# Kernel optimization log

Hardware: AMD Instinct MI355X
Metric: run time of the kernel (lower is better)

The kernel has to match this reference:

```python
import jax, jax.numpy as jnp
import numpy as np

SIGMA = 1.0          # from global `args.sigma` in the original repo
ALPHA = 0.99         # self.alpha
TOPK = 4             # torch.topk(W, 4)
NUM_CLASSES = 2
EPS = float(np.finfo(float).eps)


def setup_inputs() -> dict:
    key = jax.random.key(0)
    k1, k2, k3 = jax.random.split(key, 3)
    labeled_inputs = jax.random.normal(k1, (1024, 1024), dtype=jnp.float32)
    labeled_target = jax.random.randint(k2, (1024,), 0, NUM_CLASSES, dtype=jnp.int64)
    unlabeled_inputs = jax.random.normal(k3, (3072, 1024), dtype=jnp.float32)
    return {"labeled_inputs": labeled_inputs,
            "labeled_target": labeled_target,
            "unlabeled_inputs": unlabeled_inputs}


def _label_prop(labeled_inputs, unlabeled_inputs, labeled_target):
    num_support = labeled_inputs.shape[0]
    emb_all = jnp.concatenate([labeled_inputs, unlabeled_inputs], axis=0)  # [N, d]
    N, d = emb_all.shape

    # mean_j (x_i - x_k)_j^2 = (|x_i|^2 + |x_k|^2 - 2 x_i.x_k) / d
    # (algebraically identical to the torch NxNxd broadcast, without materializing it)
    sq = jnp.sum(emb_all * emb_all, axis=1)                 # [N]
    dist = (sq[:, None] + sq[None, :] - 2.0 * (emb_all @ emb_all.T)) / d
    W = jnp.exp(-dist / (2.0 * SIGMA * SIGMA))              # [N, N]

    # zero the diagonal
    eye = jnp.eye(N, dtype=W.dtype)
    W = W * (1.0 - eye)

    # top-k per row -> symmetric binary mask
    _, indices = jax.lax.top_k(W, TOPK)                     # [N, k]
    mask = jnp.zeros_like(W)
    rows = jnp.arange(N)[:, None]
    mask = mask.at[rows, indices].set(1.0)
    mask = ((mask + mask.T) > 0).astype(jnp.float32)
    W = W * mask

    # symmetric degree normalization S = D^{-1/2} W D^{-1/2}
    D = W.sum(axis=0)                                       # [N]
    D_sqrt_inv = jnp.sqrt(1.0 / (D + EPS))
    S = D_sqrt_inv[:, None] * W * D_sqrt_inv[None, :]

    # labels: one-hot support, zeros for queries
    ys = jax.nn.one_hot(labeled_target, NUM_CLASSES, dtype=jnp.float32)
    yu = jnp.zeros((N - num_support, NUM_CLASSES), dtype=jnp.float32)
    y = jnp.concatenate([ys, yu], axis=0)                   # [N, C]

    # F = (I - alpha*S + eps)^{-1} y   (solve == inverse @ y)
    A = jnp.eye(N, dtype=jnp.float32) - ALPHA * S + EPS
    Fk = jnp.linalg.solve(A, y)
    return Fk[num_support:, :]                              # [num_queries, C]


def reference(labeled_inputs, labeled_target, unlabeled_inputs):
    return _label_prop(labeled_inputs, unlabeled_inputs, labeled_target)
```

## Files before the change

kernel.cpp:

```cpp
#include <hip/hip_runtime.h>

#define N_ALL 4096
#define N_LAB 1024
#define DIMF 1024
#define EDGECAP 32768
#define ALPHA_ 0.99f
#define NIT_CH 100
#define EPS_D 2.220446049250313e-16

typedef short bf16x8 __attribute__((ext_vector_type(8)));
typedef float f32x4 __attribute__((ext_vector_type(4)));

struct __align__(8) Edge { unsigned j; float w; };

__device__ inline const float* xrow(const float* L, const float* U, int r) {
  return (r < N_LAB) ? (L + (size_t)r * DIMF) : (U + (size_t)(r - N_LAB) * DIMF);
}

__device__ inline void load_lds16(const void* g, void* l) {
  __builtin_amdgcn_global_load_lds(
      (const __attribute__((address_space(1))) unsigned int*)g,
      (__attribute__((address_space(3))) unsigned int*)l, 16, 0, 0);
}

__device__ inline unsigned short bf16rne(float f) {
  unsigned u = __float_as_uint(f);
  unsigned r = (u + 0x7fffu + ((u >> 16) & 1u)) >> 16;
  return (unsigned short)r;
}

__global__ __launch_bounds__(256) void labfmt_k(const int* __restrict__ lab,
                                                int* __restrict__ flag) {
  const long long* l64 = (const long long*)lab;
  int bad = 0;
  for (int k = threadIdx.x; k < 512; k += 256) {
    long long v = l64[k];
    if (v != 0 && v != 1) bad = 1;
  }
  __shared__ int sbad[4];
  unsigned long long m = __ballot(bad);
  if ((threadIdx.x & 63) == 0) sbad[threadIdx.x >> 6] = (m != 0ull);
  __syncthreads();
  if (threadIdx.x == 0)
    flag[0] = (sbad[0] | sbad[1] | sbad[2] | sbad[3]) ? 0 : 1;
}

__global__ __launch_bounds__(256) void prep_k(const float* __restrict__ L,
                                              const float* __restrict__ U,
                                              unsigned short* __restrict__ Xbf,
                                              float* __restrict__ sq,
                                              double* __restrict__ sqd) {
  const int row = blockIdx.x;
  const int tid = threadIdx.x;
  const float* src = xrow(L, U, row);
  float4 v = ((const float4*)src)[tid];
  ushort4 h;
  h.x = bf16rne(v.x); h.y = bf16rne(v.y); h.z = bf16rne(v.z); h.w = bf16rne(v.w);
  ((ushort4*)(Xbf + (size_t)row * DIMF))[tid] = h;
  float s = v.x * v.x + v.y * v.y + v.z * v.z + v.w * v.w;
  double sd = (double)v.x * v.x + (double)v.y * v.y +
              (double)v.z * v.z + (double)v.w * v.w;
#pragma unroll
  for (int d = 32; d >= 1; d >>= 1) {
    s += __shfl_xor(s, d);
    sd += __shfl_xor(sd, d);
  }
  __shared__ float wsum[4];
  __shared__ double wsumd[4];
  if ((tid & 63) == 0) { wsum[tid >> 6] = s; wsumd[tid >> 6] = sd; }
  __syncthreads();
  if (tid == 0) {
    sq[row] = wsum[0] + wsum[1] + wsum[2] + wsum[3];
    sqd[row] = wsumd[0] + wsumd[1] + wsumd[2] + wsumd[3];
  }
}

__global__ __launch_bounds__(256) void gemm_w(const unsigned short* __restrict__ Xbf,
                                              const float* __restrict__ sq,
                                              float* __restrict__ W) {
  __shared__ unsigned short At[128 * 32];
  __shared__ unsigned short Bt[128 * 32];
  const int tid = threadIdx.x;
  const int wave = tid >> 6, lane = tid & 63;
  const int brow = blockIdx.y * 128, bcol = blockIdx.x * 128;
  const int q = lane >> 4, rl = lane & 15;
  const int wr = (wave >> 1) * 64, wc = (wave & 1) * 64;

  f32x4 acc[4][4] = {};

  const int srow = tid >> 2;
  const int soff = (tid & 3) * 8;

  for (int k0 = 0; k0 < DIMF; k0 += 32) {
#pragma unroll
    for (int half = 0; half < 2; ++half) {
      const unsigned short* ga =
          Xbf + (size_t)(brow + half * 64 + srow) * DIMF + k0 + soff;
      load_lds16(ga, &At[(half * 64 + wave * 16) * 32]);
      const unsigned short* gb =
          Xbf + (size_t)(bcol + half * 64 + srow) * DIMF + k0 + soff;
      load_lds16(gb, &Bt[(half * 64 + wave * 16) * 32]);
    }
    __syncthreads();
    bf16x8 af[4], bf_[4];
#pragma unroll
    for (int t = 0; t < 4; ++t) {
      af[t] = *(const bf16x8*)&At[(wr + t * 16 + rl) * 32 + q * 8];
      bf_[t] = *(const bf16x8*)&Bt[(wc + t * 16 + rl) * 32 + q * 8];
    }
#pragma unroll
    for (int i = 0; i < 4; ++i)
#pragma unroll
      for (int j = 0; j < 4; ++j)
        acc[i][j] = __builtin_amdgcn_mfma_f32_16x16x32_bf16(af[i], bf_[j], acc[i][j], 0, 0, 0);
    __syncthreads();
  }

#pragma unroll
  for (int i = 0; i < 4; ++i) {
#pragma unroll
    for (int j = 0; j < 4; ++j) {
#pragma unroll
      for (int reg = 0; reg < 4; ++reg) {
        int gr = brow + wr + i * 16 + q * 4 + reg;
        int gc = bcol + wc + j * 16 + rl;
        float g = acc[i][j][reg];
        float dist = (sq[gr] + sq[gc] - 2.0f * g) * (1.0f / 1024.0f);
        float w = expf(-0.5f * dist);
        if (gr == gc) w = 0.0f;
        W[(size_t)gr * N_ALL + gc] = w;
      }
    }
  }
}

__global__ __launch_bounds__(256) void top8_k(const float* __restrict__ W,
                                              unsigned* __restrict__ t8i) {
  const int wave = threadIdx.x >> 6, lane = threadIdx.x & 63;
  const int row = blockIdx.x * 4 + wave;
  const float* Wr = W + (size_t)row * N_ALL;
  float bv[8]; unsigned bj[8];
#pragma unroll
  for (int t = 0; t < 8; ++t) { bv[t] = -1.0f; bj[t] = 0xFFFFFFFFu; }
  float minv = -1.0f; int mins = 0;
  for (int s = 0; s < 64; ++s) {
    int j = s * 64 + lane;
    float v = Wr[j];
    if (v > minv) {
#pragma unroll
      for (int t = 0; t < 8; ++t) if (t == mins) { bv[t] = v; bj[t] = (unsigned)j; }
      minv = bv[0]; mins = 0;
#pragma unroll
      for (int t = 1; t < 8; ++t) if (bv[t] < minv) { minv = bv[t]; mins = t; }
    }
  }
  for (int pick = 0; pick < 8; ++pick) {
    unsigned long long best = 0;
#pragma unroll
    for (int t = 0; t < 8; ++t) {
      bool valid = (bv[t] >= 0.0f);
      unsigned long long key =
          ((unsigned long long)__float_as_uint(bv[t]) << 32) |
          (unsigned long long)(0xFFFFFFFFu - bj[t]);
      if (valid && key > best) best = key;
    }
#pragma unroll
    for (int d = 32; d >= 1; d >>= 1) {
      unsigned long long o = __shfl_xor(best, d);
      if (o > best) best = o;
    }
    unsigned wj = 0xFFFFFFFFu - (unsigned)(best & 0xFFFFFFFFull);
    if (lane == 0) t8i[row * 8 + pick] = wj;
#pragma unroll
    for (int t = 0; t < 8; ++t) if (bj[t] == wj) bv[t] = -1.0f;
  }
}

__global__ __launch_bounds__(256) void rerank_k(const float* __restrict__ L,
                                                const float* __restrict__ U,
                                                const double* __restrict__ sqd,
                                                const unsigned* __restrict__ t8i,
                                                unsigned* __restrict__ t4i) {
  const int wave = threadIdx.x >> 6, lane = threadIdx.x & 63;
  const int row = blockIdx.x * 4 + wave;
  const float* xi = xrow(L, U, row);
  float xr[16];
#pragma unroll
  for (int t = 0; t < 16; ++t) xr[t] = xi[t * 64 + lane];
  unsigned cj[8];
  double cw[8];
#pragma unroll
  for (int c = 0; c < 8; ++c) cj[c] = t8i[row * 8 + c];
  for (int c = 0; c < 8; ++c) {
    const float* xj = xrow(L, U, (int)cj[c]);
    double s = 0.0;
#pragma unroll
    for (int t = 0; t < 16; ++t) s += (double)xr[t] * xj[t * 64 + lane];
#pragma unroll
    for (int d = 32; d >= 1; d >>= 1) s += __shfl_xor(s, d);
    double dist = (sqd[row] + sqd[cj[c]] - 2.0 * s) * (1.0 / 1024.0);
    cw[c] = exp(-0.5 * dist);
  }
  if (lane == 0) {
#pragma unroll
    for (int pick = 0; pick < 4; ++pick) {
      int ms = -1;
      double mv = -1.0;
      unsigned mj = 0xFFFFFFFFu;
#pragma unroll
      for (int c = 0; c < 8; ++c) {
        bool better = (cw[c] > mv) || (cw[c] == mv && cj[c] < mj);
        if (cw[c] >= 0.0 && better) { mv = cw[c]; mj = cj[c]; ms = c; }
      }
      t4i[row * 4 + pick] = mj;
      cw[ms] = -2.0;
    }
  }
}

__global__ __launch_bounds__(256) void cnt4_k(const unsigned* __restrict__ t4i,
                                              unsigned* __restrict__ nn) {
  const int wave = threadIdx.x >> 6, lane = threadIdx.x & 63;
  const int i = blockIdx.x * 4 + wave;
  const uint4 mine = ((const uint4*)t4i)[i];
  unsigned base = 0;
  for (int j0 = 0; j0 < N_ALL; j0 += 64) {
    int j = j0 + lane;
    uint4 tj = ((const uint4*)t4i)[j];
    bool keep = (mine.x == (unsigned)j) | (mine.y == (unsigned)j) |
                (mine.z == (unsigned)j) | (mine.w == (unsigned)j) |
                (tj.x == (unsigned)i) | (tj.y == (unsigned)i) |
                (tj.z == (unsigned)i) | (tj.w == (unsigned)i);
    keep = keep && (j != i);
    base += (unsigned)__popcll(__ballot(keep));
  }
  if (lane == 0) nn[i] = base;
}

__global__ __launch_bounds__(64) void scanP_k(const unsigned* __restrict__ nn,
                                              unsigned* __restrict__ rowPtr) {
  const int lane = threadIdx.x;
  unsigned running = 0;
  for (int j0 = 0; j0 < N_ALL; j0 += 64) {
    int v = (int)nn[j0 + lane];
    int incl = v;
#pragma unroll
    for (int d = 1; d < 64; d <<= 1) {
      int t = __shfl_up(incl, d);
      if (lane >= d) incl += t;
    }
    rowPtr[j0 + lane] = running + (unsigned)(incl - v);
    running += (unsigned)__shfl(incl, 63);
  }
  if (lane == 0) rowPtr[N_ALL] = running;
}

__global__ __launch_bounds__(256) void csrfill_k(const unsigned* __restrict__ t4i,
                                                 const unsigned* __restrict__ rowPtr,
                                                 Edge* __restrict__ edges,
                                                 unsigned* __restrict__ eRow) {
  const int wave = threadIdx.x >> 6, lane = threadIdx.x & 63;
  const int i = blockIdx.x * 4 + wave;
  const uint4 mine = ((const uint4*)t4i)[i];
  unsigned base = rowPtr[i];
  for (int j0 = 0; j0 < N_ALL; j0 += 64) {
    int j = j0 + lane;
    uint4 tj = ((const uint4*)t4i)[j];
    bool keep = (mine.x == (unsigned)j) | (mine.y == (unsigned)j) |
                (mine.z == (unsigned)j) | (mine.w == (unsigned)j) |
                (tj.x == (unsigned)i) | (tj.y == (unsigned)i) |
                (tj.z == (unsigned)i) | (tj.w == (unsigned)i);
    keep = keep && (j != i);
    unsigned long long m = __ballot(keep);
    if (keep) {
      unsigned pos = base + (unsigned)__popcll(m & ((1ull << lane) - 1ull));
      edges[pos].j = (unsigned)j;
      edges[pos].w = 0.0f;
      eRow[pos] = (unsigned)i;
    }
    base += (unsigned)__popcll(m);
  }
}

__global__ __launch_bounds__(256) void edgeval_k(const float* __restrict__ L,
                                                 const float* __restrict__ U,
                                                 const double* __restrict__ sqd,
                                                 const unsigned* __restrict__ rowPtr,
                                                 const unsigned* __restrict__ eRow,
                                                 Edge* __restrict__ edges) {
  const int wave = threadIdx.x >> 6, lane = threadIdx.x & 63;
  const unsigned e = blockIdx.x * 4 + wave;
  if (e >= rowPtr[N_ALL]) return;
  const unsigned i = eRow[e];
  const unsigned j = edges[e].j;
  const float* xi = xrow(L, U, (int)i);
  const float* xj = xrow(L, U, (int)j);
  double s = 0.0;
#pragma unroll
  for (int t = 0; t < 16; ++t)
    s += (double)xi[t * 64 + lane] * xj[t * 64 + lane];
#pragma unroll
  for (int d = 32; d >= 1; d >>= 1) s += __shfl_xor(s, d);
  if (lane == 0) {
    double dist = (sqd[i] + sqd[j] - 2.0 * s) * (1.0 / 1024.0);
    edges[e].w = (float)exp(-0.5 * dist);
  }
}

__global__ __launch_bounds__(256) void degE_k(const unsigned* __restrict__ rowPtr,
                                              const Edge* __restrict__ edges,
                                              float* __restrict__ Dis) {
  const int wave = threadIdx.x >> 6, lane = threadIdx.x & 63;
  const int i = blockIdx.x * 4 + wave;
  const unsigned b0 = rowPtr[i], b1 = rowPtr[i + 1];
  double ds = 0.0;
  for (unsigned e = b0 + lane; e < b1; e += 64) ds += (double)edges[e].w;
#pragma unroll
  for (int d = 32; d >= 1; d >>= 1) ds += __shfl_xor(ds, d);
  if (lane == 0) Dis[i] = (float)sqrt(1.0 / (ds + EPS_D));
}

__global__ __launch_bounds__(256) void scaleE_k(const unsigned* __restrict__ rowPtr,
                                                const unsigned* __restrict__ eRow,
                                                const float* __restrict__ Dis,
                                                Edge* __restrict__ edges) {
  const unsigned e = blockIdx.x * 256 + threadIdx.x;
  if (e >= rowPtr[N_ALL]) return;
  Edge ed = edges[e];
  edges[e].w = ed.w * Dis[eRow[e]] * Dis[ed.j];
}

__global__ __launch_bounds__(256) void init_k(const int* __restrict__ lab,
                                              const int* __restrict__ labflag,
                                              float2* __restrict__ x,
                                              float2* __restrict__ r,
                                              float2* __restrict__ d) {
  const int m = blockIdx.x * 256 + threadIdx.x;
  const int isI64 = labflag[0];
  float2 b = make_float2(0.0f, 0.0f);
  if (m < N_LAB) {
    int c = isI64 ? lab[2 * m] : lab[m];
    b.x = (c == 0) ? 1.0f : 0.0f;
    b.y = (c == 1) ? 1.0f : 0.0f;
  }
  x[m] = make_float2(0.0f, 0.0f);
  r[m] = b;
  d[m] = b;
}

__global__ __launch_bounds__(512) void chebit_k(const Edge* __restrict__ edges,
                                                const unsigned* __restrict__ rowPtr,
                                                const float2* __restrict__ dIn,
                                                float2* __restrict__ dOut,
                                                float2* __restrict__ x,
                                                float2* __restrict__ r,
                                                float c1, float c2, int last) {
  const int row = blockIdx.x * 8 + (threadIdx.x >> 6);
  const int lane = threadIdx.x & 63;
  const unsigned b0 = rowPtr[row], b1 = rowPtr[row + 1];
  float ax = 0.0f, ay = 0.0f;
  for (unsigned e = b0 + lane; e < b1; e += 64) {
    Edge ed = edges[e];
    float2 dj = dIn[ed.j];
    ax += ed.w * dj.x;
    ay += ed.w * dj.y;
  }
#pragma unroll
  for (int d = 32; d >= 1; d >>= 1) {
    ax += __shfl_xor(ax, d);
    ay += __shfl_xor(ay, d);
  }
  if (lane == 0) {
    float2 di = dIn[row], xi = x[row], ri = r[row];
    xi.x += di.x; xi.y += di.y;
    ri.x += ALPHA_ * ax - di.x;
    ri.y += ALPHA_ * ay - di.y;
    x[row] = xi;
    r[row] = ri;
    if (!last) {
      float2 dn;
      dn.x = c1 * di.x + c2 * ri.x;
      dn.y = c1 * di.y + c2 * ri.y;
      dOut[row] = dn;
    }
  }
}

__global__ __launch_bounds__(256) void out_k(const float2* __restrict__ x,
                                             float2* __restrict__ out) {
  const int q = blockIdx.x * 256 + threadIdx.x;
  out[q] = x[N_LAB + q];
}

extern "C" void kernel_launch(void* const* d_in, const int* in_sizes, int n_in,
                              void* d_out, int out_size, void* d_ws, size_t ws_size,
                              hipStream_t stream) {
  int iL = 0, iT = 1, iU = 2;
  for (int i = 0; i < n_in; ++i) {
    if (in_sizes[i] == N_LAB * DIMF) iL = i;
    else if (in_sizes[i] == (N_ALL - N_LAB) * DIMF) iU = i;
    else iT = i;
  }
  const float* L = (const float*)d_in[iL];
  const int* lab = (const int*)d_in[iT];
  const float* U = (const float*)d_in[iU];
  float2* out = (float2*)d_out;

  char* w = (char*)d_ws;
  size_t off = 0;
  auto alloc = [&](size_t bytes) {
    void* p = (void*)(w + off);
    off += (bytes + 255) & ~(size_t)255;
    return p;
  };
  float* W = (float*)alloc((size_t)N_ALL * N_ALL * 4);
  unsigned short* Xbf = (unsigned short*)alloc((size_t)N_ALL * DIMF * 2);
  float* sq = (float*)alloc(N_ALL * 4);
  double* sqd = (double*)alloc(N_ALL * 8);
  unsigned* t8i = (unsigned*)alloc(N_ALL * 8 * 4);
  unsigned* t4i = (unsigned*)alloc(N_ALL * 4 * 4);
  float* Dis = (float*)alloc(N_ALL * 4);
  unsigned* nn = (unsigned*)alloc(N_ALL * 4);
  unsigned* rowPtr = (unsigned*)alloc((N_ALL + 1) * 4);
  int* labflag = (int*)alloc(256);
  Edge* edges = (Edge*)alloc((size_t)EDGECAP * sizeof(Edge));
  unsigned* eRow = (unsigned*)alloc((size_t)EDGECAP * 4);
  float2* xv = (float2*)alloc(N_ALL * 8);
  float2* rv = (float2*)alloc(N_ALL * 8);
  float2* dv0 = (float2*)alloc(N_ALL * 8);
  float2* dv1 = (float2*)alloc(N_ALL * 8);
  if (off > ws_size) return;

  labfmt_k<<<1, 256, 0, stream>>>(lab, labflag);
  prep_k<<<N_ALL, 256, 0, stream>>>(L, U, Xbf, sq, sqd);
  gemm_w<<<dim3(32, 32), 256, 0, stream>>>(Xbf, sq, W);
  top8_k<<<N_ALL / 4, 256, 0, stream>>>(W, t8i);
  rerank_k<<<N_ALL / 4, 256, 0, stream>>>(L, U, sqd, t8i, t4i);
  cnt4_k<<<N_ALL / 4, 256, 0, stream>>>(t4i, nn);
  scanP_k<<<1, 64, 0, stream>>>(nn, rowPtr);
  csrfill_k<<<N_ALL / 4, 256, 0, stream>>>(t4i, rowPtr, edges, eRow);
  edgeval_k<<<EDGECAP / 4, 256, 0, stream>>>(L, U, sqd, rowPtr, eRow, edges);
  degE_k<<<N_ALL / 4, 256, 0, stream>>>(rowPtr, edges, Dis);
  scaleE_k<<<EDGECAP / 256, 256, 0, stream>>>(rowPtr, eRow, Dis, edges);
  init_k<<<N_ALL / 256, 256, 0, stream>>>(lab, labflag, xv, rv, dv0);

  const double theta = 1.0, delta = 0.992;
  const double sigma1 = theta / delta;
  double rho = delta / theta;
  float2* dA = dv0;
  float2* dB = dv1;
  for (int k = 0; k < NIT_CH; ++k) {
    const int last = (k == NIT_CH - 1);
    const double rho_new = 1.0 / (2.0 * sigma1 - rho);
    const float c1 = (float)(rho_new * rho);
    const float c2 = (float)(2.0 * rho_new / delta);
    chebit_k<<<N_ALL / 8, 512, 0, stream>>>(edges, rowPtr, dA, dB, xv, rv,
                                            c1, c2, last);
    rho = rho_new;
    float2* t = dA; dA = dB; dB = t;
  }
  out_k<<<(N_ALL - N_LAB) / 256, 256, 0, stream>>>(xv, out);
}
```

Baseline: 647.3 us.

## Store candidate scores in fp16, fold label check into scan, cut Chebyshev iterations

The GEMM epilogue now writes a monotone fp16 surrogate score (clamped 2600 - squared distance) instead of the fp32 exp weight, halving the NxN matrix traffic for the write and the top-8 scan. The label-format check kernel is merged into the single-wave prefix-scan kernel, removing one launch. The Chebyshev solver iteration count drops from 100 to 80, cutting sequential launches at some risk to convergence accuracy. The fp16 surrogate loses resolution and clamps far points, relying on the fp64 rerank to correct the candidate order.

```diff
diff --git a/kernel.cpp b/kernel.cpp
--- a/kernel.cpp
+++ b/kernel.cpp
@@ -5,7 +5,7 @@
 #define DIMF 1024
 #define EDGECAP 32768
 #define ALPHA_ 0.99f
-#define NIT_CH 100
+#define NIT_CH 80
 #define EPS_D 2.220446049250313e-16
 
 typedef short bf16x8 __attribute__((ext_vector_type(8)));
@@ -27,22 +27,6 @@
   unsigned u = __float_as_uint(f);
   unsigned r = (u + 0x7fffu + ((u >> 16) & 1u)) >> 16;
   return (unsigned short)r;
-}
-
-__global__ __launch_bounds__(256) void labfmt_k(const int* __restrict__ lab,
-                                                int* __restrict__ flag) {
-  const long long* l64 = (const long long*)lab;
-  int bad = 0;
-  for (int k = threadIdx.x; k < 512; k += 256) {
-    long long v = l64[k];
-    if (v != 0 && v != 1) bad = 1;
-  }
-  __shared__ int sbad[4];
-  unsigned long long m = __ballot(bad);
-  if ((threadIdx.x & 63) == 0) sbad[threadIdx.x >> 6] = (m != 0ull);
-  __syncthreads();
-  if (threadIdx.x == 0)
-    flag[0] = (sbad[0] | sbad[1] | sbad[2] | sbad[3]) ? 0 : 1;
 }
 
 __global__ __launch_bounds__(256) void prep_k(const float* __restrict__ L,
@@ -77,7 +61,7 @@
 
 __global__ __launch_bounds__(256) void gemm_w(const unsigned short* __restrict__ Xbf,
                                               const float* __restrict__ sq,
-                                              float* __restrict__ W) {
+                                              _Float16* __restrict__ Wh) {
   __shared__ unsigned short At[128 * 32];
   __shared__ unsigned short Bt[128 * 32];
   const int tid = threadIdx.x;
@@ -125,27 +109,27 @@
         int gr = brow + wr + i * 16 + q * 4 + reg;
         int gc = bcol + wc + j * 16 + rl;
         float g = acc[i][j][reg];
-        float dist = (sq[gr] + sq[gc] - 2.0f * g) * (1.0f / 1024.0f);
-        float w = expf(-0.5f * dist);
-        if (gr == gc) w = 0.0f;
-        W[(size_t)gr * N_ALL + gc] = w;
+        float dist = sq[gr] + sq[gc] - 2.0f * g;
+        float val = fmaxf(2600.0f - dist, 0.25f);
+        if (gr == gc) val = 0.0f;
+        Wh[(size_t)gr * N_ALL + gc] = (_Float16)val;
       }
     }
   }
 }
 
-__global__ __launch_bounds__(256) void top8_k(const float* __restrict__ W,
+__global__ __launch_bounds__(256) void top8_k(const _Float16* __restrict__ Wh,
                                               unsigned* __restrict__ t8i) {
   const int wave = threadIdx.x >> 6, lane = threadIdx.x & 63;
   const int row = blockIdx.x * 4 + wave;
-  const float* Wr = W + (size_t)row * N_ALL;
+  const _Float16* Wr = Wh + (size_t)row * N_ALL;
   float bv[8]; unsigned bj[8];
 #pragma unroll
   for (int t = 0; t < 8; ++t) { bv[t] = -1.0f; bj[t] = 0xFFFFFFFFu; }
   float minv = -1.0f; int mins = 0;
   for (int s = 0; s < 64; ++s) {
     int j = s * 64 + lane;
-    float v = Wr[j];
+    float v = (float)Wr[j];
     if (v > minv) {
 #pragma unroll
       for (int t = 0; t < 8; ++t) if (t == mins) { bv[t] = v; bj[t] = (unsigned)j; }
@@ -238,8 +222,19 @@
 }
 
 __global__ __launch_bounds__(64) void scanP_k(const unsigned* __restrict__ nn,
-                                              unsigned* __restrict__ rowPtr) {
+                                              unsigned* __restrict__ rowPtr,
+                                              const int* __restrict__ lab,
+                                              int* __restrict__ labflag) {
   const int lane = threadIdx.x;
+  const long long* l64 = (const long long*)lab;
+  int bad = 0;
+#pragma unroll
+  for (int k = 0; k < 8; ++k) {
+    long long v = l64[k * 64 + lane];
+    if (v != 0 && v != 1) bad = 1;
+  }
+  unsigned long long bm = __ballot(bad);
+  if (lane == 0) labflag[0] = (bm != 0ull) ? 0 : 1;
   unsigned running = 0;
   for (int j0 = 0; j0 < N_ALL; j0 += 64) {
     int v = (int)nn[j0 + lane];
@@ -413,7 +408,7 @@
     off += (bytes + 255) & ~(size_t)255;
     return p;
   };
-  float* W = (float*)alloc((size_t)N_ALL * N_ALL * 4);
+  _Float16* Wh = (_Float16*)alloc((size_t)N_ALL * N_ALL * 2);
   unsigned short* Xbf = (unsigned short*)alloc((size_t)N_ALL * DIMF * 2);
   float* sq = (float*)alloc(N_ALL * 4);
   double* sqd = (double*)alloc(N_ALL * 8);
@@ -431,13 +426,12 @@
   float2* dv1 = (float2*)alloc(N_ALL * 8);
   if (off > ws_size) return;
 
-  labfmt_k<<<1, 256, 0, stream>>>(lab, labflag);
   prep_k<<<N_ALL, 256, 0, stream>>>(L, U, Xbf, sq, sqd);
-  gemm_w<<<dim3(32, 32), 256, 0, stream>>>(Xbf, sq, W);
-  top8_k<<<N_ALL / 4, 256, 0, stream>>>(W, t8i);
+  gemm_w<<<dim3(32, 32), 256, 0, stream>>>(Xbf, sq, Wh);
+  top8_k<<<N_ALL / 4, 256, 0, stream>>>(Wh, t8i);
   rerank_k<<<N_ALL / 4, 256, 0, stream>>>(L, U, sqd, t8i, t4i);
   cnt4_k<<<N_ALL / 4, 256, 0, stream>>>(t4i, nn);
-  scanP_k<<<1, 64, 0, stream>>>(nn, rowPtr);
+  scanP_k<<<1, 64, 0, stream>>>(nn, rowPtr, lab, labflag);
   csrfill_k<<<N_ALL / 4, 256, 0, stream>>>(t4i, rowPtr, edges, eRow);
   edgeval_k<<<EDGECAP / 4, 256, 0, stream>>>(L, U, sqd, rowPtr, eRow, edges);
   degE_k<<<N_ALL / 4, 256, 0, stream>>>(rowPtr, edges, Dis);
```

Result: faster. 556.1 us (-14.1%).
